# Kernel tuning notes

Hardware: AMD Instinct MI355X
Metric: run time of the kernel (lower is better)

The kernel has to match this reference:

```python
import jax, jax.numpy as jnp
import numpy as np

# --- quantization helpers (I-BERT-style symmetric quantization) ---

def _quant_int(x, scale, bit):
    # round(x/scale) clamped to signed `bit`-bit range (SymmetricQuantFunction)
    n = 2 ** (bit - 1) - 1
    return jnp.clip(jnp.round(x / scale), -n - 1, n)


def quant_linear(x, s_x, W, b, weight_bit=8):
    """QuantLinear: per-output-channel symmetric 8-bit weight quant, int GEMM, dequant.
    Returns (output, bias_scaling_factor[out_features])."""
    n = 2 ** (weight_bit - 1) - 1
    w_scale = jnp.maximum(jnp.max(jnp.abs(W), axis=1), 1e-8) / n          # (out,)
    w_int = _quant_int(W, w_scale[:, None], weight_bit)                   # int-valued (out,in)
    b_scale = w_scale * s_x                                               # (out,) broadcasts with scalar s_x
    b_int = jnp.round(b / b_scale)                                        # 32-bit bias, no clamp needed
    x_int = x / s_x                                                       # int-valued activations
    out_int = jnp.einsum('bsi,oi->bso', x_int, w_int) + b_int
    return out_int * b_scale, b_scale


def quant_act(x, bit):
    """QuantAct: per-tensor symmetric requantization to `bit` bits (dynamic min/max)."""
    n = 2 ** (bit - 1) - 1
    scale = jnp.maximum(jnp.max(jnp.abs(x)), 1e-8) / n                    # scalar
    x_int = _quant_int(x, scale, bit)
    return x_int * scale, scale


def int_gelu(x, s):
    """IntGELU (I-BERT): integer 2nd-order polynomial approximation of erf."""
    k = 1.4142
    c0, c1 = -0.2888, -1.769
    c2 = 1.0 / c0
    SHIFT = 14  # 'const' in the original code

    x_int = x / s
    se = s / k  # scaling factor fed to int_erf
    # --- int_erf ---
    b_int = jnp.floor(c1 / se)
    c_int = jnp.floor(c2 / se ** 2)
    sign = jnp.sign(x_int)
    abs_int = jnp.minimum(jnp.abs(x_int), -b_int)
    y_int = sign * ((abs_int + b_int) ** 2 + c_int)
    se2 = se ** 2 * c0
    y_int = jnp.floor(y_int / 2 ** SHIFT)
    se2 = se2 * 2 ** SHIFT
    # --- gelu = x * (erf/2 + 1/2) in integer form ---
    shift_int = jnp.floor(1.0 / se2)
    out_int = x_int * (y_int + shift_int)
    s_out = s * se2 / 2
    return out_int * s_out, s_out


def setup_inputs() -> dict:
    key = jax.random.key(0)
    k_x, k_w1, k_b1, k_w2, k_b2 = jax.random.split(key, 5)
    B, S, D, H = 8, 1024, 768, 3072
    x = jax.random.normal(k_x, (B, S, D), dtype=jnp.float32)
    act_scaling_factor = jnp.full((1,), 0.02, dtype=jnp.float32)
    # pre-quantize x onto its input grid (x arrives already quantized in the real pipeline)
    x = jnp.round(x / act_scaling_factor) * act_scaling_factor
    W1 = jax.random.normal(k_w1, (H, D), dtype=jnp.float32) * 0.02
    b1 = jax.random.normal(k_b1, (H,), dtype=jnp.float32) * 0.02
    W2 = jax.random.normal(k_w2, (D, H), dtype=jnp.float32) * 0.02
    b2 = jax.random.normal(k_b2, (D,), dtype=jnp.float32) * 0.02
    return {"x": x, "act_scaling_factor": act_scaling_factor,
            "W1": W1, "b1": b1, "W2": W2, "b2": b2}


def reference(x, act_scaling_factor, W1, b1, W2, b2):
    s = act_scaling_factor
    h, s = quant_linear(x, s, W1, b1)       # fc1: int8 GEMM + dequant
    h, s = quant_act(h, 8)                  # qact_gelu
    h, s = int_gelu(h, s)                   # IntGELU
    h, s = quant_act(h, 8)                  # qact1 (drop=0.0 -> identity)
    h, s = quant_linear(h, s, W2, b2)       # fc2
    h, s = quant_act(h, 16)                 # qact2 (16-bit)
    return h, s
```

## Files before the change

kernel.cpp:

```cpp
#include <hip/hip_runtime.h>

typedef _Float16 half8  __attribute__((ext_vector_type(8)));
typedef _Float16 half4v __attribute__((ext_vector_type(4)));
typedef float f32x4 __attribute__((ext_vector_type(4)));
typedef int int4v __attribute__((ext_vector_type(4)));

#define M_DIM 8192
#define D_DIM 768
#define H_DIM 3072

#define WS_WSCALE2   16
#define WS_BINT1     (WS_WSCALE2 + 768*4)
#define WS_BSCALE1   (WS_BINT1 + 3072*4)
#define WS_XQ        34560UL
#define WS_WQ1       (WS_XQ  + (size_t)M_DIM*D_DIM*2)
#define WS_WQ2I      (WS_WQ1 + (size_t)H_DIM*D_DIM*2)
#define WS_H1        (WS_WQ2I + (size_t)D_DIM*H_DIM)
#define WS_Q2        WS_H1
#define WS_H2        (WS_H1 + (size_t)M_DIM*H_DIM)
#define WS_Q1        (WS_H1 + (size_t)M_DIM*H_DIM*4)

__device__ __forceinline__ void gl_lds16(const _Float16* g, _Float16* l) {
  __builtin_amdgcn_global_load_lds(
      (const __attribute__((address_space(1))) void*)g,
      (__attribute__((address_space(3))) void*)l, 16, 0, 0);
}
__device__ __forceinline__ void gl_lds16c(const char* g, char* l) {
  __builtin_amdgcn_global_load_lds(
      (const __attribute__((address_space(1))) void*)g,
      (__attribute__((address_space(3))) void*)l, 16, 0, 0);
}

struct GeluP { float scale1, bintg, cintg, shiftint, s_out; };

__device__ __forceinline__ GeluP gelu_params(float max1) {
  GeluP p;
  p.scale1 = fmaxf(max1, 1e-8f) / 127.0f;
  float se = p.scale1 / 1.4142f;
  p.bintg = floorf(-1.769f / se);
  p.cintg = floorf(((float)(1.0 / -0.2888)) / (se * se));
  float se2 = ((se * se) * -0.2888f) * 16384.0f;
  p.shiftint = floorf(1.0f / se2);
  p.s_out = (p.scale1 * se2) * 0.5f;
  return p;
}

__device__ __forceinline__ float gelu_val(const GeluP& p, float qf) {
  float sg = (qf > 0.f) ? 1.f : ((qf < 0.f) ? -1.f : 0.f);
  float aq = fminf(fabsf(qf), -p.bintg);
  float t = aq + p.bintg;
  float y = sg * (t * t + p.cintg);
  float yf = floorf(y * (1.0f / 16384.0f));
  return (qf * (yf + p.shiftint)) * p.s_out;
}

__global__ __launch_bounds__(256)
void k12_prep(const float* __restrict__ W1, const float* __restrict__ b1,
              const float* __restrict__ W2, const float* __restrict__ x,
              const float* __restrict__ sxp,
              _Float16* __restrict__ wq1, char* __restrict__ wq2i,
              float* __restrict__ wscale2, float* __restrict__ bint1,
              float* __restrict__ bscale1, _Float16* __restrict__ xq,
              unsigned* __restrict__ wsu)
{
  if (blockIdx.x == 0 && threadIdx.x == 0) { wsu[0] = 0u; wsu[1] = 0u; wsu[2] = 0u; }
  if (blockIdx.x < 960) {
    int w = blockIdx.x * 4 + (threadIdx.x >> 6);
    int lane = threadIdx.x & 63;
    if (w < H_DIM) {
      const float* row = W1 + (size_t)w * D_DIM;
      f32x4 v[3]; float m = 0.f;
#pragma unroll
      for (int t = 0; t < 3; t++) {
        v[t] = *(const f32x4*)(row + t * 256 + lane * 4);
#pragma unroll
        for (int j = 0; j < 4; j++) m = fmaxf(m, fabsf(v[t][j]));
      }
#pragma unroll
      for (int off = 32; off >= 1; off >>= 1) m = fmaxf(m, __shfl_xor(m, off));
      float wsc = fmaxf(m, 1e-8f) / 127.0f;
      _Float16* orow = wq1 + (size_t)w * D_DIM;
#pragma unroll
      for (int t = 0; t < 3; t++) {
        half4v h;
#pragma unroll
        for (int j = 0; j < 4; j++) {
          float q = fminf(fmaxf(rintf(v[t][j] / wsc), -128.f), 127.f);
          h[j] = (_Float16)q;
        }
        *(half4v*)(orow + t * 256 + lane * 4) = h;
      }
      if (lane == 0) {
        float bs = wsc * sxp[0];
        bint1[w] = rintf(b1[w] / bs);
        bscale1[w] = bs;
      }
    } else {
      int o = w - H_DIM;
      const float* row = W2 + (size_t)o * H_DIM;
      f32x4 v[12]; float m = 0.f;
#pragma unroll
      for (int t = 0; t < 12; t++) {
        v[t] = *(const f32x4*)(row + t * 256 + lane * 4);
#pragma unroll
        for (int j = 0; j < 4; j++) m = fmaxf(m, fabsf(v[t][j]));
      }
#pragma unroll
      for (int off = 32; off >= 1; off >>= 1) m = fmaxf(m, __shfl_xor(m, off));
      float wsc = fmaxf(m, 1e-8f) / 127.0f;
      unsigned* orow = (unsigned*)(wq2i + (size_t)o * H_DIM);
#pragma unroll
      for (int t = 0; t < 12; t++) {
        unsigned pk = 0;
#pragma unroll
        for (int j = 0; j < 4; j++) {
          float q = fminf(fmaxf(rintf(v[t][j] / wsc), -128.f), 127.f);
          pk |= ((unsigned)(unsigned char)(char)(int)q) << (8 * j);
        }
        orow[t * 64 + lane] = pk;
      }
      if (lane == 0) wscale2[o] = wsc;
    }
  } else {
    float sx = sxp[0];
    const int n4 = (M_DIM * D_DIM) / 4;
    const int stride = 1024 * 256;
    for (int i = (blockIdx.x - 960) * 256 + threadIdx.x; i < n4; i += stride) {
      f32x4 v = ((const f32x4*)x)[i];
      half4v h;
#pragma unroll
      for (int j = 0; j < 4; j++) h[j] = (_Float16)(v[j] / sx);
      ((half4v*)xq)[i] = h;
    }
  }
}

__global__ __launch_bounds__(512)
void gemm_f16_dp(const _Float16* __restrict__ A, const _Float16* __restrict__ B,
                 const float* __restrict__ bint, const float* __restrict__ bscale,
                 float* __restrict__ C, unsigned* __restrict__ maxw, int N, int K)
{
  __shared__ _Float16 lds[3 * 10240];
  __shared__ float wred[8];
  const int tid = threadIdx.x;
  const int wid = tid >> 6;
  const int lane = tid & 63;
  const int m0 = blockIdx.x * 128;
  const int n0 = blockIdx.y * 192;
  const int wm = wid >> 2;
  const int wn = wid & 3;

  const bool w4 = (wid < 4);
  const int nL = w4 ? 3 : 2;
  const int g0 = w4 ? 3 * wid : 12 + 2 * (wid - 4);
  const int sri = lane >> 2;
  const int cs  = (lane & 3) ^ ((lane >> 3) & 3);
  const _Float16* srcp[3];
#pragma unroll
  for (int i = 0; i < 3; i++) {
    if (i < nL) {
      const int cr = (g0 + i) * 16 + sri;
      srcp[i] = (cr < 128 ? A + (size_t)(m0 + cr) * K
                          : B + (size_t)(n0 + cr - 128) * K) + cs * 8;
    } else srcp[i] = nullptr;
  }

#define STAGE_DP(t, s) do {                                                  \
    _Float16* const base = lds + (size_t)(s) * 10240;                        \
    _Pragma("unroll")                                                        \
    for (int i = 0; i < 3; i++)                                              \
      if (i < nL) gl_lds16(srcp[i] + (size_t)(t) * 32, base + (g0 + i) * 512); \
  } while (0)

  const int ks = lane >> 4;
  const int swc = (ks ^ (((lane & 15) >> 1) & 3)) * 16;
  int aoff[4], boff[3];
#pragma unroll
  for (int f = 0; f < 4; f++)
    aoff[f] = (wm * 64 + f * 16 + (lane & 15)) * 64 + swc;
#pragma unroll
  for (int f = 0; f < 3; f++)
    boff[f] = 8192 + (wn * 48 + f * 16 + (lane & 15)) * 64 + swc;

  f32x4 acc[4][3];
#pragma unroll
  for (int i = 0; i < 4; i++)
#pragma unroll
    for (int j = 0; j < 3; j++) acc[i][j] = (f32x4){0.f, 0.f, 0.f, 0.f};

  const int nt = K / 32;
  STAGE_DP(0, 0);
  STAGE_DP(1, 1);
  for (int t = 0; t < nt; ++t) {
    const int s = t % 3;
    if (t + 1 < nt) {
      if (w4) asm volatile("s_waitcnt vmcnt(3)" ::: "memory");
      else    asm volatile("s_waitcnt vmcnt(2)" ::: "memory");
    } else    asm volatile("s_waitcnt vmcnt(0)" ::: "memory");
    asm volatile("s_barrier" ::: "memory");
    if (t + 2 < nt) STAGE_DP(t + 2, (t + 2) % 3);
    const char* sb = (const char*)(lds + (size_t)s * 10240);
    half8 a[4], b[3];
#pragma unroll
    for (int f = 0; f < 4; f++) a[f] = *(const half8*)(sb + aoff[f]);
#pragma unroll
    for (int f = 0; f < 3; f++) b[f] = *(const half8*)(sb + boff[f]);
    __builtin_amdgcn_s_setprio(1);
#pragma unroll
    for (int i = 0; i < 4; i++)
#pragma unroll
      for (int j = 0; j < 3; j++)
        acc[i][j] = __builtin_amdgcn_mfma_f32_16x16x32_f16(a[i], b[j], acc[i][j], 0, 0, 0);
    __builtin_amdgcn_s_setprio(0);
  }
#undef STAGE_DP

  float tmax = 0.f;
  const int orow0 = m0 + wm * 64 + (lane >> 4) * 4;
  const int ocol0 = n0 + wn * 48 + (lane & 15);
#pragma unroll
  for (int j = 0; j < 3; j++) {
    const int col = ocol0 + j * 16;
    const float bi = bint[col];
    const float bs = bscale[col];
#pragma unroll
    for (int i = 0; i < 4; i++) {
#pragma unroll
      for (int e = 0; e < 4; e++) {
        const int rowm = orow0 + i * 16 + e;
        float v = (acc[i][j][e] + bi) * bs;
        C[(size_t)rowm * N + col] = v;
        tmax = fmaxf(tmax, fabsf(v));
      }
    }
  }
#pragma unroll
  for (int off = 32; off >= 1; off >>= 1) tmax = fmaxf(tmax, __shfl_xor(tmax, off));
  if (lane == 0) wred[wid] = tmax;
  __syncthreads();
  if (tid == 0) {
    float bm = 0.f;
#pragma unroll
    for (int i = 0; i < 8; i++) bm = fmaxf(bm, wred[i]);
    atomicMax(maxw, __float_as_uint(bm));
  }
}

__global__ __launch_bounds__(256)
void k4_gelu(const float* __restrict__ h1, const unsigned* __restrict__ wsu,
             char* __restrict__ q1, unsigned* __restrict__ maxw, int n4)
{
  GeluP p = gelu_params(__uint_as_float(wsu[0]));
  float tmax = 0.f;
  int stride = gridDim.x * blockDim.x;
  for (int i = blockIdx.x * blockDim.x + threadIdx.x; i < n4; i += stride) {
    f32x4 h = ((const f32x4*)h1)[i];
    unsigned pack = 0;
#pragma unroll
    for (int j = 0; j < 4; j++) {
      float qf = fminf(fmaxf(rintf(h[j] / p.scale1), -128.f), 127.f);
      tmax = fmaxf(tmax, fabsf(gelu_val(p, qf)));
      pack |= ((unsigned)(unsigned char)(char)(int)qf) << (8 * j);
    }
    ((unsigned*)q1)[i] = pack;
  }
#pragma unroll
  for (int off = 32; off >= 1; off >>= 1) tmax = fmaxf(tmax, __shfl_xor(tmax, off));
  __shared__ float wred[4];
  int wid = threadIdx.x >> 6;
  if ((threadIdx.x & 63) == 0) wred[wid] = tmax;
  __syncthreads();
  if (threadIdx.x == 0) {
    float bm = fmaxf(fmaxf(wred[0], wred[1]), fmaxf(wred[2], wred[3]));
    atomicMax(maxw, __float_as_uint(bm));
  }
}

__global__ __launch_bounds__(256)
void k5_q2(const char* __restrict__ q1, const unsigned* __restrict__ wsu,
           char* __restrict__ q2, int n16)
{
  GeluP p = gelu_params(__uint_as_float(wsu[0]));
  float scale2 = fmaxf(__uint_as_float(wsu[1]), 1e-8f) / 127.0f;
  int stride = gridDim.x * blockDim.x;
  for (int i = blockIdx.x * blockDim.x + threadIdx.x; i < n16; i += stride) {
    uint4 pk = ((const uint4*)q1)[i];
    uint4 o;
    unsigned* pw[4] = {&o.x, &o.y, &o.z, &o.w};
    unsigned pr[4] = {pk.x, pk.y, pk.z, pk.w};
#pragma unroll
    for (int w = 0; w < 4; w++) {
      unsigned acc = 0;
#pragma unroll
      for (int j = 0; j < 4; j++) {
        float qf = (float)(int)(signed char)(pr[w] >> (8 * j));
        float g = gelu_val(p, qf);
        float q2f = fminf(fmaxf(rintf(g / scale2), -128.f), 127.f);
        acc |= ((unsigned)(unsigned char)(char)(int)q2f) << (8 * j);
      }
      *pw[w] = acc;
    }
    ((uint4*)q2)[i] = o;
  }
}

#define I8_SLOT 16384

__global__ __launch_bounds__(256)
void gemm_i8_dp(const char* __restrict__ A, const char* __restrict__ B,
                const unsigned* __restrict__ wsu, const float* __restrict__ wscale2,
                const float* __restrict__ b2, float* __restrict__ C,
                unsigned* __restrict__ maxw, int N, int K)
{
  __shared__ char lds[3 * I8_SLOT];
  __shared__ float wred[4];
  const int tid = threadIdx.x;
  const int w = tid >> 6;
  const int l = tid & 63;
  const int m0 = blockIdx.x * 64;
  const int n0 = blockIdx.y * 192;
  const float scale2 = fmaxf(__uint_as_float(wsu[1]), 1e-8f) / 127.0f;

  const int sri = l >> 2;
  const int csw = (l & 3) ^ ((l >> 3) & 3);
  const char* pa  = A + (size_t)(m0 + w * 16 + sri) * K + csw * 16;
  const char* pbg = B + (size_t)(n0 + 48 * w + sri) * K + csw * 16;

#define STAGE_I(t, s) do {                                                   \
    char* const base = lds + (size_t)(s) * I8_SLOT;                          \
    gl_lds16c(pa + (size_t)(t) * 64,                    base + w * 1024);    \
    gl_lds16c(pbg + (size_t)(t) * 64,                   base + 4096 + (3*w) * 1024);     \
    gl_lds16c(pbg + (size_t)16 * K + (size_t)(t) * 64,  base + 4096 + (3*w+1) * 1024);   \
    gl_lds16c(pbg + (size_t)32 * K + (size_t)(t) * 64,  base + 4096 + (3*w+2) * 1024);   \
  } while (0)

  const int ks = l >> 4;
  const int swc = (ks ^ (((l & 15) >> 1) & 3)) * 16;
  int aoff[4], boff[3];
#pragma unroll
  for (int f = 0; f < 4; f++)
    aoff[f] = (f * 16 + (l & 15)) * 64 + swc;
#pragma unroll
  for (int f = 0; f < 3; f++)
    boff[f] = 4096 + ((3 * w + f) * 16 + (l & 15)) * 64 + swc;

  int4v acc[4][3];
#pragma unroll
  for (int i = 0; i < 4; i++)
#pragma unroll
    for (int j = 0; j < 3; j++) acc[i][j] = (int4v){0, 0, 0, 0};

  const int nt = K / 64;
  STAGE_I(0, 0);
  STAGE_I(1, 1);
  for (int t = 0; t < nt; ++t) {
    const int s = t % 3;
    if (t + 1 < nt) asm volatile("s_waitcnt vmcnt(4)" ::: "memory");
    else            asm volatile("s_waitcnt vmcnt(0)" ::: "memory");
    asm volatile("s_barrier" ::: "memory");
    if (t + 2 < nt) STAGE_I(t + 2, (t + 2) % 3);
    const char* sb = lds + (size_t)s * I8_SLOT;
    int4v a[4], b[3];
#pragma unroll
    for (int f = 0; f < 4; f++) a[f] = *(const int4v*)(sb + aoff[f]);
#pragma unroll
    for (int f = 0; f < 3; f++) b[f] = *(const int4v*)(sb + boff[f]);
    __builtin_amdgcn_s_setprio(1);
#pragma unroll
    for (int i = 0; i < 4; i++)
#pragma unroll
      for (int j = 0; j < 3; j++)
        acc[i][j] = __builtin_amdgcn_mfma_i32_16x16x64_i8(a[i], b[j], acc[i][j], 0, 0, 0);
    __builtin_amdgcn_s_setprio(0);
  }
#undef STAGE_I

  float tmax = 0.f;
  const int orow0 = m0 + (l >> 4) * 4;
  const int ocol0 = n0 + w * 48 + (l & 15);
#pragma unroll
  for (int j = 0; j < 3; j++) {
    const int col = ocol0 + j * 16;
    const float bs = wscale2[col] * scale2;
    const float bi = rintf(b2[col] / bs);
#pragma unroll
    for (int i = 0; i < 4; i++) {
#pragma unroll
      for (int e = 0; e < 4; e++) {
        const int rowm = orow0 + i * 16 + e;
        float v = ((float)acc[i][j][e] + bi) * bs;
        C[(size_t)rowm * N + col] = v;
        tmax = fmaxf(tmax, fabsf(v));
      }
    }
  }
#pragma unroll
  for (int off = 32; off >= 1; off >>= 1) tmax = fmaxf(tmax, __shfl_xor(tmax, off));
  if (l == 0) wred[w] = tmax;
  __syncthreads();
  if (tid == 0) {
    float bm = fmaxf(fmaxf(wred[0], wred[1]), fmaxf(wred[2], wred[3]));
    atomicMax(maxw, __float_as_uint(bm));
  }
}

__global__ __launch_bounds__(256)
void k7_final(const float* __restrict__ h2, const unsigned* __restrict__ wsu,
              float* __restrict__ out, int n4, int ntot)
{
  float scale16 = fmaxf(__uint_as_float(wsu[2]), 1e-8f) / 32767.0f;
  int stride = gridDim.x * blockDim.x;
  for (int i = blockIdx.x * blockDim.x + threadIdx.x; i < n4; i += stride) {
    f32x4 v = ((const f32x4*)h2)[i];
    f32x4 o;
#pragma unroll
    for (int j = 0; j < 4; j++) {
      float q = fminf(fmaxf(rintf(v[j] / scale16), -32768.f), 32767.f);
      o[j] = q * scale16;
    }
    ((f32x4*)out)[i] = o;
  }
  if (blockIdx.x == 0 && threadIdx.x == 0) out[ntot] = scale16;
}

extern "C" void kernel_launch(void* const* d_in, const int* in_sizes, int n_in,
                              void* d_out, int out_size, void* d_ws, size_t ws_size,
                              hipStream_t stream)
{
  (void)in_sizes; (void)n_in; (void)out_size; (void)ws_size;
  const float* x  = (const float*)d_in[0];
  const float* sx = (const float*)d_in[1];
  const float* W1 = (const float*)d_in[2];
  const float* b1 = (const float*)d_in[3];
  const float* W2 = (const float*)d_in[4];
  const float* b2 = (const float*)d_in[5];
  float* out = (float*)d_out;
  char* ws = (char*)d_ws;

  unsigned* wsu   = (unsigned*)ws;
  float* wscale2  = (float*)(ws + WS_WSCALE2);
  float* bint1    = (float*)(ws + WS_BINT1);
  float* bscale1  = (float*)(ws + WS_BSCALE1);
  _Float16* xq    = (_Float16*)(ws + WS_XQ);
  _Float16* wq1   = (_Float16*)(ws + WS_WQ1);
  char* wq2i      = (char*)(ws + WS_WQ2I);
  float* h1       = (float*)(ws + WS_H1);
  char* q2        = (char*)(ws + WS_Q2);
  float* h2       = (float*)(ws + WS_H2);
  char* q1        = (char*)(ws + WS_Q1);

  k12_prep<<<dim3(1984), dim3(256), 0, stream>>>(W1, b1, W2, x, sx, wq1, wq2i,
                                                 wscale2, bint1, bscale1, xq, wsu);
  gemm_f16_dp<<<dim3(64, 16), dim3(512), 0, stream>>>(xq, wq1, bint1, bscale1, h1, wsu + 0, H_DIM, D_DIM);
  k4_gelu<<<dim3(2048), dim3(256), 0, stream>>>(h1, wsu, q1, wsu + 1, (M_DIM * H_DIM) / 4);
  k5_q2<<<dim3(2048), dim3(256), 0, stream>>>(q1, wsu, q2, (M_DIM * H_DIM) / 16);
  gemm_i8_dp<<<dim3(128, 4), dim3(256), 0, stream>>>(q2, wq2i, wsu, wscale2, b2, h2, wsu + 2, D_DIM, H_DIM);
  k7_final<<<dim3(2048), dim3(256), 0, stream>>>(h2, wsu, out, (M_DIM * D_DIM) / 4, M_DIM * D_DIM);
}
```

Measured before the change: 180.4 us.

## Fuse GELU requant passes and final 16-bit quant using in-kernel grid barriers

Merges the two elementwise GELU/requant kernels into one persistent kernel that keeps the int8 codes in registers across a software grid barrier, and folds the final 16-bit requantization into the int8 GEMM epilogue behind a second grid barrier. This drops the q1 and h2 intermediate round trips through global memory and two kernel launches. The cost is that all blocks must be co-resident (1024 blocks at occupancy 4 and 512 GEMM blocks at occupancy 3); if they are not, the barrier deadlocks. Blocks also idle while spinning at each barrier.

```diff
diff --git a/kernel.cpp b/kernel.cpp
--- a/kernel.cpp
+++ b/kernel.cpp
@@ -9,16 +9,14 @@
 #define D_DIM 768
 #define H_DIM 3072
 
-#define WS_WSCALE2   16
+#define WS_WSCALE2   64
 #define WS_BINT1     (WS_WSCALE2 + 768*4)
 #define WS_BSCALE1   (WS_BINT1 + 3072*4)
-#define WS_XQ        34560UL
+#define WS_XQ        34624UL
 #define WS_WQ1       (WS_XQ  + (size_t)M_DIM*D_DIM*2)
 #define WS_WQ2I      (WS_WQ1 + (size_t)H_DIM*D_DIM*2)
 #define WS_H1        (WS_WQ2I + (size_t)D_DIM*H_DIM)
 #define WS_Q2        WS_H1
-#define WS_H2        (WS_H1 + (size_t)M_DIM*H_DIM)
-#define WS_Q1        (WS_H1 + (size_t)M_DIM*H_DIM*4)
 
 __device__ __forceinline__ void gl_lds16(const _Float16* g, _Float16* l) {
   __builtin_amdgcn_global_load_lds(
@@ -54,6 +52,16 @@
   return (qf * (yf + p.shiftint)) * p.s_out;
 }
 
+__device__ __forceinline__ void grid_bar(unsigned* ctr, unsigned nblk) {
+  __syncthreads();
+  if (threadIdx.x == 0) {
+    __threadfence();
+    atomicAdd(ctr, 1u);
+    while (atomicAdd(ctr, 0u) < nblk) __builtin_amdgcn_s_sleep(8);
+  }
+  __syncthreads();
+}
+
 __global__ __launch_bounds__(256)
 void k12_prep(const float* __restrict__ W1, const float* __restrict__ b1,
               const float* __restrict__ W2, const float* __restrict__ x,
@@ -63,7 +71,7 @@
               float* __restrict__ bscale1, _Float16* __restrict__ xq,
               unsigned* __restrict__ wsu)
 {
-  if (blockIdx.x == 0 && threadIdx.x == 0) { wsu[0] = 0u; wsu[1] = 0u; wsu[2] = 0u; }
+  if (blockIdx.x == 0 && threadIdx.x < 8) wsu[threadIdx.x] = 0u;
   if (blockIdx.x < 960) {
     int w = blockIdx.x * 4 + (threadIdx.x >> 6);
     int lane = threadIdx.x & 63;
@@ -246,80 +254,73 @@
   }
 }
 
-__global__ __launch_bounds__(256)
-void k4_gelu(const float* __restrict__ h1, const unsigned* __restrict__ wsu,
-             char* __restrict__ q1, unsigned* __restrict__ maxw, int n4)
+__global__ __launch_bounds__(256, 4)
+void k45g(const float* __restrict__ h1, unsigned* __restrict__ wsu,
+          char* __restrict__ q2)
 {
-  GeluP p = gelu_params(__uint_as_float(wsu[0]));
+  __shared__ float wred[4];
+  __shared__ float s_scale2;
+  GeluP p = gelu_params(__uint_as_float(atomicAdd(&wsu[0], 0u)));
+  const int tid = threadIdx.x;
+  const size_t base = (size_t)blockIdx.x * (24 * 256) + tid;
+  unsigned code[24];
   float tmax = 0.f;
-  int stride = gridDim.x * blockDim.x;
-  for (int i = blockIdx.x * blockDim.x + threadIdx.x; i < n4; i += stride) {
-    f32x4 h = ((const f32x4*)h1)[i];
-    unsigned pack = 0;
+#pragma unroll
+  for (int i = 0; i < 24; i++) {
+    f32x4 h = ((const f32x4*)h1)[base + i * 256];
+    unsigned pk = 0;
 #pragma unroll
     for (int j = 0; j < 4; j++) {
       float qf = fminf(fmaxf(rintf(h[j] / p.scale1), -128.f), 127.f);
       tmax = fmaxf(tmax, fabsf(gelu_val(p, qf)));
-      pack |= ((unsigned)(unsigned char)(char)(int)qf) << (8 * j);
-    }
-    ((unsigned*)q1)[i] = pack;
+      pk |= ((unsigned)(unsigned char)(char)(int)qf) << (8 * j);
+    }
+    code[i] = pk;
   }
 #pragma unroll
   for (int off = 32; off >= 1; off >>= 1) tmax = fmaxf(tmax, __shfl_xor(tmax, off));
-  __shared__ float wred[4];
-  int wid = threadIdx.x >> 6;
-  if ((threadIdx.x & 63) == 0) wred[wid] = tmax;
-  __syncthreads();
-  if (threadIdx.x == 0) {
+  if ((tid & 63) == 0) wred[tid >> 6] = tmax;
+  __syncthreads();
+  if (tid == 0) {
     float bm = fmaxf(fmaxf(wred[0], wred[1]), fmaxf(wred[2], wred[3]));
-    atomicMax(maxw, __float_as_uint(bm));
-  }
-}
-
-__global__ __launch_bounds__(256)
-void k5_q2(const char* __restrict__ q1, const unsigned* __restrict__ wsu,
-           char* __restrict__ q2, int n16)
-{
-  GeluP p = gelu_params(__uint_as_float(wsu[0]));
-  float scale2 = fmaxf(__uint_as_float(wsu[1]), 1e-8f) / 127.0f;
-  int stride = gridDim.x * blockDim.x;
-  for (int i = blockIdx.x * blockDim.x + threadIdx.x; i < n16; i += stride) {
-    uint4 pk = ((const uint4*)q1)[i];
-    uint4 o;
-    unsigned* pw[4] = {&o.x, &o.y, &o.z, &o.w};
-    unsigned pr[4] = {pk.x, pk.y, pk.z, pk.w};
-#pragma unroll
-    for (int w = 0; w < 4; w++) {
-      unsigned acc = 0;
-#pragma unroll
-      for (int j = 0; j < 4; j++) {
-        float qf = (float)(int)(signed char)(pr[w] >> (8 * j));
-        float g = gelu_val(p, qf);
-        float q2f = fminf(fmaxf(rintf(g / scale2), -128.f), 127.f);
-        acc |= ((unsigned)(unsigned char)(char)(int)q2f) << (8 * j);
-      }
-      *pw[w] = acc;
-    }
-    ((uint4*)q2)[i] = o;
+    atomicMax(&wsu[1], __float_as_uint(bm));
+  }
+  grid_bar(&wsu[4], 1024u);
+  if (tid == 0)
+    s_scale2 = fmaxf(__uint_as_float(atomicAdd(&wsu[1], 0u)), 1e-8f) / 127.0f;
+  __syncthreads();
+  const float scale2 = s_scale2;
+#pragma unroll
+  for (int i = 0; i < 24; i++) {
+    unsigned pk = code[i], o = 0;
+#pragma unroll
+    for (int j = 0; j < 4; j++) {
+      float qf = (float)(int)(signed char)(pk >> (8 * j));
+      float g = gelu_val(p, qf);
+      float q2f = fminf(fmaxf(rintf(g / scale2), -128.f), 127.f);
+      o |= ((unsigned)(unsigned char)(char)(int)q2f) << (8 * j);
+    }
+    ((unsigned*)q2)[base + i * 256] = o;
   }
 }
 
 #define I8_SLOT 16384
 
-__global__ __launch_bounds__(256)
-void gemm_i8_dp(const char* __restrict__ A, const char* __restrict__ B,
-                const unsigned* __restrict__ wsu, const float* __restrict__ wscale2,
-                const float* __restrict__ b2, float* __restrict__ C,
-                unsigned* __restrict__ maxw, int N, int K)
+__global__ __launch_bounds__(256, 3)
+void gemm_i8_g(const char* __restrict__ A, const char* __restrict__ B,
+               unsigned* __restrict__ wsu, const float* __restrict__ wscale2,
+               const float* __restrict__ b2, float* __restrict__ out,
+               int N, int K, int ntot)
 {
   __shared__ char lds[3 * I8_SLOT];
   __shared__ float wred[4];
+  __shared__ float s_scale16;
   const int tid = threadIdx.x;
   const int w = tid >> 6;
   const int l = tid & 63;
   const int m0 = blockIdx.x * 64;
   const int n0 = blockIdx.y * 192;
-  const float scale2 = fmaxf(__uint_as_float(wsu[1]), 1e-8f) / 127.0f;
+  const float scale2 = fmaxf(__uint_as_float(atomicAdd(&wsu[1], 0u)), 1e-8f) / 127.0f;
 
   const int sri = l >> 2;
   const int csw = (l & 3) ^ ((l >> 3) & 3);
@@ -384,43 +385,42 @@
     const float bs = wscale2[col] * scale2;
     const float bi = rintf(b2[col] / bs);
 #pragma unroll
+    for (int i = 0; i < 4; i++)
+#pragma unroll
+      for (int e = 0; e < 4; e++)
+        tmax = fmaxf(tmax, fabsf(((float)acc[i][j][e] + bi) * bs));
+  }
+#pragma unroll
+  for (int off = 32; off >= 1; off >>= 1) tmax = fmaxf(tmax, __shfl_xor(tmax, off));
+  if (l == 0) wred[w] = tmax;
+  __syncthreads();
+  if (tid == 0) {
+    float bm = fmaxf(fmaxf(wred[0], wred[1]), fmaxf(wred[2], wred[3]));
+    atomicMax(&wsu[2], __float_as_uint(bm));
+  }
+  grid_bar(&wsu[5], 512u);
+  if (tid == 0)
+    s_scale16 = fmaxf(__uint_as_float(atomicAdd(&wsu[2], 0u)), 1e-8f) / 32767.0f;
+  __syncthreads();
+  const float scale16 = s_scale16;
+
+#pragma unroll
+  for (int j = 0; j < 3; j++) {
+    const int col = ocol0 + j * 16;
+    const float bs = wscale2[col] * scale2;
+    const float bi = rintf(b2[col] / bs);
+#pragma unroll
     for (int i = 0; i < 4; i++) {
 #pragma unroll
       for (int e = 0; e < 4; e++) {
         const int rowm = orow0 + i * 16 + e;
         float v = ((float)acc[i][j][e] + bi) * bs;
-        C[(size_t)rowm * N + col] = v;
-        tmax = fmaxf(tmax, fabsf(v));
-      }
-    }
-  }
-#pragma unroll
-  for (int off = 32; off >= 1; off >>= 1) tmax = fmaxf(tmax, __shfl_xor(tmax, off));
-  if (l == 0) wred[w] = tmax;
-  __syncthreads();
-  if (tid == 0) {
-    float bm = fmaxf(fmaxf(wred[0], wred[1]), fmaxf(wred[2], wred[3]));
-    atomicMax(maxw, __float_as_uint(bm));
-  }
-}
-
-__global__ __launch_bounds__(256)
-void k7_final(const float* __restrict__ h2, const unsigned* __restrict__ wsu,
-              float* __restrict__ out, int n4, int ntot)
-{
-  float scale16 = fmaxf(__uint_as_float(wsu[2]), 1e-8f) / 32767.0f;
-  int stride = gridDim.x * blockDim.x;
-  for (int i = blockIdx.x * blockDim.x + threadIdx.x; i < n4; i += stride) {
-    f32x4 v = ((const f32x4*)h2)[i];
-    f32x4 o;
-#pragma unroll
-    for (int j = 0; j < 4; j++) {
-      float q = fminf(fmaxf(rintf(v[j] / scale16), -32768.f), 32767.f);
-      o[j] = q * scale16;
-    }
-    ((f32x4*)out)[i] = o;
-  }
-  if (blockIdx.x == 0 && threadIdx.x == 0) out[ntot] = scale16;
+        float q = fminf(fmaxf(rintf(v / scale16), -32768.f), 32767.f);
+        out[(size_t)rowm * N + col] = q * scale16;
+      }
+    }
+  }
+  if (blockIdx.x == 0 && blockIdx.y == 0 && tid == 0) out[ntot] = scale16;
 }
 
 extern "C" void kernel_launch(void* const* d_in, const int* in_sizes, int n_in,
@@ -446,14 +446,10 @@
   char* wq2i      = (char*)(ws + WS_WQ2I);
   float* h1       = (float*)(ws + WS_H1);
   char* q2        = (char*)(ws + WS_Q2);
-  float* h2       = (float*)(ws + WS_H2);
-  char* q1        = (char*)(ws + WS_Q1);
 
   k12_prep<<<dim3(1984), dim3(256), 0, stream>>>(W1, b1, W2, x, sx, wq1, wq2i,
                                                  wscale2, bint1, bscale1, xq, wsu);
   gemm_f16_dp<<<dim3(64, 16), dim3(512), 0, stream>>>(xq, wq1, bint1, bscale1, h1, wsu + 0, H_DIM, D_DIM);
-  k4_gelu<<<dim3(2048), dim3(256), 0, stream>>>(h1, wsu, q1, wsu + 1, (M_DIM * H_DIM) / 4);
-  k5_q2<<<dim3(2048), dim3(256), 0, stream>>>(q1, wsu, q2, (M_DIM * H_DIM) / 16);
-  gemm_i8_dp<<<dim3(128, 4), dim3(256), 0, stream>>>(q2, wq2i, wsu, wscale2, b2, h2, wsu + 2, D_DIM, H_DIM);
-  k7_final<<<dim3(2048), dim3(256), 0, stream>>>(h2, wsu, out, (M_DIM * D_DIM) / 4, M_DIM * D_DIM);
-}
+  k45g<<<dim3(1024), dim3(256), 0, stream>>>(h1, wsu, q2);
+  gemm_i8_g<<<dim3(128, 4), dim3(256), 0, stream>>>(q2, wq2i, wsu, wscale2, b2, out, D_DIM, H_DIM, M_DIM * D_DIM);
+}
```

Measured after the change: 301.4 us. 67.1% more time.
